# Kernel tuning notes

Measured on AMD Instinct MI355X. Metric: run time of the kernel, lower is better.

The kernel has to match this reference:

```python
import jax, jax.numpy as jnp
import numpy as np

B, C, N = 32, 1024, 512
OUTDIM = 256
EPS_SQRT = 1e-12   # clamp before sqrt so diagonal zeros stay differentiable
EPS_NORM = 1e-12   # torch F.normalize eps


def setup_inputs() -> dict:
    key = jax.random.key(0)
    k1, k2, k3, k4, k5 = jax.random.split(key, 5)
    xi = jax.random.normal(k1, (B, 256, N), dtype=jnp.float32)
    xh = jax.random.normal(k2, (B, 256, N), dtype=jnp.float32)
    xo = jax.random.normal(k3, (B, C, N), dtype=jnp.float32)
    # LazyLinear(outdim) materializes as Linear(N*N, outdim)
    fan_in = N * N
    bound = 1.0 / np.sqrt(fan_in)
    W = jax.random.uniform(k4, (fan_in, OUTDIM), dtype=jnp.float32, minval=-bound, maxval=bound)
    b = jax.random.uniform(k5, (OUTDIM,), dtype=jnp.float32, minval=-bound, maxval=bound)
    return {"xi": xi, "xh": xh, "xo": xo, "W": W, "b": b}


def reference(xi, xh, xo, W, b):
    # xi, xh are unused by SoGA.forward
    x = jnp.transpose(xo, (0, 2, 1))                 # [B, N, C]
    # similarity (Gram) matrix over points
    S = jnp.einsum('bnc,bmc->bnm', x, x)             # [B, N, N], symmetric
    # pairwise Euclidean distance between rows of S
    sq = jnp.sum(S * S, axis=-1)                     # [B, N]
    G = jnp.einsum('bnk,bmk->bnm', S, S)             # [B, N, N]
    d2 = sq[:, :, None] + sq[:, None, :] - 2.0 * G
    D = jnp.sqrt(jnp.maximum(d2, EPS_SQRT))          # [B, N, N]
    flat = D.reshape(D.shape[0], -1)                 # [B, N*N]
    d_out = flat @ W + b                             # [B, outdim]
    norm = jnp.maximum(jnp.linalg.norm(d_out, axis=-1, keepdims=True), EPS_NORM)
    return d_out / norm
```

## Files before the change

### kernel.cpp

```cpp
#include <hip/hip_runtime.h>

typedef unsigned short ushort_t;
typedef __attribute__((ext_vector_type(8))) unsigned short ushort8;
typedef __attribute__((ext_vector_type(4))) unsigned short ushort4v;
typedef __attribute__((ext_vector_type(8))) __bf16 bf16x8;
typedef __attribute__((ext_vector_type(4))) float f32x4;
typedef __attribute__((ext_vector_type(4))) float f4;

#define B_ 32
#define C_ 1024
#define N_ 512
#define O_ 256

__device__ inline float bf2f(unsigned short u) {
  unsigned int i = ((unsigned int)u) << 16;
  return __builtin_bit_cast(float, i);
}
__device__ inline unsigned short f2bf(float f) {
  unsigned int i = __builtin_bit_cast(unsigned int, f);
  i += 0x7FFFu + ((i >> 16) & 1u);
  return (unsigned short)(i >> 16);
}

__device__ inline void gl_lds16(const ushort_t* g, ushort_t* l) {
  __builtin_amdgcn_global_load_lds(
      (const __attribute__((address_space(1))) void*)g,
      (__attribute__((address_space(3))) void*)l, 16, 0, 0);
}

__global__ __launch_bounds__(256) void k_transpose(const float* __restrict__ xo,
                                                   ushort_t* __restrict__ xoT) {
  __shared__ float tile[64][65];
  const int tn = blockIdx.x, tc = blockIdx.y, b = blockIdx.z;
  const int c0 = tc * 64, n0 = tn * 64;
  const int t = threadIdx.x;
  const int tr = t >> 4, tq = t & 15;
  const float* src = xo + ((size_t)b * C_ + c0) * N_ + n0;
#pragma unroll
  for (int p = 0; p < 4; ++p) {
    int c = p * 16 + tr;
    f4 v = *(const f4*)(src + (size_t)c * N_ + tq * 4);
    tile[c][tq * 4 + 0] = v[0];
    tile[c][tq * 4 + 1] = v[1];
    tile[c][tq * 4 + 2] = v[2];
    tile[c][tq * 4 + 3] = v[3];
  }
  __syncthreads();
  ushort_t* dst = xoT + ((size_t)b * N_ + n0) * C_ + c0;
#pragma unroll
  for (int p = 0; p < 4; ++p) {
    int n = p * 16 + tr;
    ushort4v u;
#pragma unroll
    for (int j = 0; j < 4; ++j) u[j] = f2bf(tile[tq * 4 + j][n]);
    *(ushort4v*)(dst + (size_t)n * C_ + tq * 4) = u;
  }
}

template <int KSTEPS, int LDK>
__device__ inline void gemm_main(const ushort_t* __restrict__ Arows,
                                 const ushort_t* __restrict__ Brows,
                                 ushort_t* lds_a, ushort_t* lds_b,
                                 f32x4 (&acc)[4][4], int t) {
  const int lane = t & 63, w = t >> 6;
  const int wr = w >> 1, wc = w & 1;
  const int l16 = lane & 15, lg = lane >> 4;
  const int srow_a = w * 32 + (lane >> 2);
  const int skp = (lane & 3) * 8;
  for (int s = 0; s < KSTEPS; ++s) {
#pragma unroll
    for (int j = 0; j < 2; ++j) {
      const int row = srow_a + j * 16;
      gl_lds16(Arows + (size_t)row * LDK + s * 32 + skp,
               lds_a + (w * 2 + j) * 512);
      gl_lds16(Brows + (size_t)row * LDK + s * 32 + skp,
               lds_b + (w * 2 + j) * 512);
    }
    __syncthreads();
    ushort8 au[4], bu[4];
#pragma unroll
    for (int i = 0; i < 4; ++i) {
      au[i] = *(const ushort8*)&lds_a[(wr * 64 + i * 16 + l16) * 32 + lg * 8];
      bu[i] = *(const ushort8*)&lds_b[(wc * 64 + i * 16 + l16) * 32 + lg * 8];
    }
#pragma unroll
    for (int ai = 0; ai < 4; ++ai)
#pragma unroll
      for (int bi = 0; bi < 4; ++bi)
        acc[ai][bi] = __builtin_amdgcn_mfma_f32_16x16x32_bf16(
            __builtin_bit_cast(bf16x8, au[ai]), __builtin_bit_cast(bf16x8, bu[bi]),
            acc[ai][bi], 0, 0, 0);
    __syncthreads();
  }
}

__global__ __launch_bounds__(256, 2) void k_sgemm(const ushort_t* __restrict__ xoT,
                                                  ushort_t* __restrict__ S) {
  __shared__ ushort_t lds_a[128 * 32];
  __shared__ ushort_t lds_b[128 * 32];
  const int b = blockIdx.y, tile = blockIdx.x;
  const int n0 = (tile >> 2) * 128, m0 = (tile & 3) * 128;
  const ushort_t* Ab = xoT + (size_t)b * N_ * C_ + (size_t)n0 * C_;
  const ushort_t* Bb = xoT + (size_t)b * N_ * C_ + (size_t)m0 * C_;
  f32x4 acc[4][4] = {};
  gemm_main<C_ / 32, C_>(Ab, Bb, lds_a, lds_b, acc, threadIdx.x);
  const int t = threadIdx.x;
  const int lane = t & 63, w = t >> 6, wr = w >> 1, wc = w & 1;
  const int l16 = lane & 15, lg = lane >> 4;
  ushort_t* Sb = S + (size_t)b * N_ * N_;
#pragma unroll
  for (int ai = 0; ai < 4; ++ai)
#pragma unroll
    for (int bi = 0; bi < 4; ++bi)
#pragma unroll
      for (int j = 0; j < 4; ++j) {
        int n = n0 + wr * 64 + ai * 16 + lg * 4 + j;
        int m = m0 + wc * 64 + bi * 16 + l16;
        Sb[(size_t)n * N_ + m] = f2bf(acc[ai][bi][j]);
      }
}

__global__ __launch_bounds__(256) void k_sq(const ushort_t* __restrict__ S,
                                            float* __restrict__ sq) {
  const int row = blockIdx.x * 4 + (threadIdx.x >> 6);
  const int lane = threadIdx.x & 63;
  ushort8 v = *(const ushort8*)(S + (size_t)row * N_ + lane * 8);
  float q = 0.f;
#pragma unroll
  for (int j = 0; j < 8; ++j) {
    float f = bf2f(v[j]);
    q += f * f;
  }
#pragma unroll
  for (int off = 32; off; off >>= 1) q += __shfl_down(q, off, 64);
  if (lane == 0) sq[row] = q;
}

__global__ __launch_bounds__(256, 2) void k_dgemm(const ushort_t* __restrict__ S,
                                                  const float* __restrict__ sq,
                                                  ushort_t* __restrict__ D) {
  __shared__ ushort_t lds_a[128 * 32];
  __shared__ ushort_t lds_b[128 * 32];
  __shared__ float sqn[128], sqm[128];
  const int b = blockIdx.y, tile = blockIdx.x;
  const int n0 = (tile >> 2) * 128, m0 = (tile & 3) * 128;
  const int t = threadIdx.x;
  if (t < 128)
    sqn[t] = sq[b * N_ + n0 + t];
  else
    sqm[t - 128] = sq[b * N_ + m0 + (t - 128)];
  const ushort_t* Ab = S + (size_t)b * N_ * N_ + (size_t)n0 * N_;
  const ushort_t* Bb = S + (size_t)b * N_ * N_ + (size_t)m0 * N_;
  f32x4 acc[4][4] = {};
  gemm_main<N_ / 32, N_>(Ab, Bb, lds_a, lds_b, acc, t);
  const int lane = t & 63, w = t >> 6, wr = w >> 1, wc = w & 1;
  const int l16 = lane & 15, lg = lane >> 4;
  ushort_t* Db = D + (size_t)b * N_ * N_;
#pragma unroll
  for (int ai = 0; ai < 4; ++ai)
#pragma unroll
    for (int bi = 0; bi < 4; ++bi)
#pragma unroll
      for (int j = 0; j < 4; ++j) {
        int nl = wr * 64 + ai * 16 + lg * 4 + j;
        int ml = wc * 64 + bi * 16 + l16;
        float d2 = sqn[nl] + sqm[ml] - 2.f * acc[ai][bi][j];
        Db[(size_t)(n0 + nl) * N_ + (m0 + ml)] = f2bf(sqrtf(fmaxf(d2, 1e-12f)));
      }
}

__global__ __launch_bounds__(256, 2) void k_dw(const ushort_t* __restrict__ Dm,
                                               const float* __restrict__ W,
                                               float* __restrict__ partial) {
  __shared__ ushort_t lds_d[32 * 512];
  const int g = blockIdx.x, t = threadIdx.x;
  const int k0 = g * 512;
#pragma unroll
  for (int i = 0; i < 8; ++i) {
    int c = i * 256 + t;
    *(ushort8*)&lds_d[c * 8] =
        *(const ushort8*)(Dm + (size_t)(c >> 6) * (N_ * N_) + k0 + (c & 63) * 8);
  }
  __syncthreads();
  const int ks = t >> 6;
  const int ob = (t & 63) * 4;
  float acc[32][4] = {};
  const float* Wb = W + ((size_t)(k0 + ks * 128)) * O_ + ob;
  const ushort_t* dbase = &lds_d[ks * 128];
  f4 wA[8], wB[8];
#define LOADW(dst, kb_)                                                      \
  {                                                                          \
    _Pragma("unroll") for (int r = 0; r < 8; ++r) dst[r] =                   \
        *(const f4*)(Wb + (size_t)((kb_)*8 + r) * O_);                       \
  }
#define COMP(kb_, w_)                                                        \
  {                                                                          \
    const int kl = (kb_)*8;                                                  \
    _Pragma("unroll") for (int bb = 0; bb < 32; ++bb) {                      \
      ushort8 dv = *(const ushort8*)&dbase[bb * 512 + kl];                   \
      _Pragma("unroll") for (int r = 0; r < 8; ++r) {                        \
        float dr = bf2f(dv[r]);                                              \
        acc[bb][0] += dr * w_[r][0];                                         \
        acc[bb][1] += dr * w_[r][1];                                         \
        acc[bb][2] += dr * w_[r][2];                                         \
        acc[bb][3] += dr * w_[r][3];                                         \
      }                                                                      \
    }                                                                        \
  }
  LOADW(wA, 0)
#pragma unroll 1
  for (int kb = 0; kb < 16; kb += 2) {
    LOADW(wB, kb + 1)
    COMP(kb, wA)
    if (kb + 2 < 16) LOADW(wA, kb + 2)
    COMP(kb + 1, wB)
  }
#undef LOADW
#undef COMP
  __syncthreads();
  float* lds_f = (float*)lds_d;
  const int lane = t & 63;
#pragma unroll
  for (int c = 0; c < 4; ++c) {
#pragma unroll
    for (int q = 0; q < 8; ++q) {
      f4 v;
      v[0] = acc[c * 8 + q][0];
      v[1] = acc[c * 8 + q][1];
      v[2] = acc[c * 8 + q][2];
      v[3] = acc[c * 8 + q][3];
      *(f4*)&lds_f[(ks * 8 + q) * 256 + lane * 4] = v;
    }
    __syncthreads();
    {
      const int q2 = t >> 5, o = (t & 31) * 8;
      f4 s0 = {}, s1 = {};
#pragma unroll
      for (int k2 = 0; k2 < 4; ++k2) {
        f4 a0 = *(const f4*)&lds_f[(k2 * 8 + q2) * 256 + o];
        f4 a1 = *(const f4*)&lds_f[(k2 * 8 + q2) * 256 + o + 4];
        s0 += a0;
        s1 += a1;
      }
      float* P = partial + ((size_t)g * B_ + c * 8 + q2) * O_ + o;
      *(f4*)P = s0;
      *(f4*)(P + 4) = s1;
    }
    __syncthreads();
  }
}

__global__ __launch_bounds__(256) void k_red1(const float* __restrict__ partial,
                                              float* __restrict__ p2) {
  const int pg = blockIdx.x, b = blockIdx.y, t = threadIdx.x;
  float s = 0.f;
#pragma unroll 8
  for (int p = pg * 64; p < pg * 64 + 64; ++p)
    s += partial[((size_t)p * B_ + b) * O_ + t];
  p2[((size_t)pg * B_ + b) * O_ + t] = s;
}

__global__ __launch_bounds__(256) void k_red2(const float* __restrict__ p2,
                                              const float* __restrict__ bias,
                                              float* __restrict__ out) {
  const int b = blockIdx.x, t = threadIdx.x;
  float s = 0.f;
#pragma unroll
  for (int pg = 0; pg < 8; ++pg) s += p2[((size_t)pg * B_ + b) * O_ + t];
  s += bias[t];
  float q = s * s;
#pragma unroll
  for (int off = 32; off; off >>= 1) q += __shfl_down(q, off, 64);
  __shared__ float lds[4];
  if ((t & 63) == 0) lds[t >> 6] = q;
  __syncthreads();
  float tot = lds[0] + lds[1] + lds[2] + lds[3];
  out[b * O_ + t] = s / fmaxf(sqrtf(tot), 1e-12f);
}

extern "C" void kernel_launch(void* const* d_in, const int* in_sizes, int n_in,
                              void* d_out, int out_size, void* d_ws, size_t ws_size,
                              hipStream_t stream) {
  const float* xo = (const float*)d_in[2];
  const float* W = (const float*)d_in[3];
  const float* bias = (const float*)d_in[4];
  float* out = (float*)d_out;

  char* ws = (char*)d_ws;
  const size_t OFF_S = 33554432, OFF_D = 50331648, OFF_SQ = 67108864,
               OFF_P2 = 67174400, NEED = 67436544;
  if (ws_size < NEED) return;
  ushort_t* xoT = (ushort_t*)ws;
  ushort_t* S = (ushort_t*)(ws + OFF_S);
  ushort_t* D = (ushort_t*)(ws + OFF_D);
  float* sq = (float*)(ws + OFF_SQ);
  float* p2 = (float*)(ws + OFF_P2);
  float* partial = (float*)ws;

  hipLaunchKernelGGL(k_transpose, dim3(8, 16, 32), dim3(256), 0, stream, xo, xoT);
  hipLaunchKernelGGL(k_sgemm, dim3(16, 32), dim3(256), 0, stream, xoT, S);
  hipLaunchKernelGGL(k_sq, dim3(4096), dim3(256), 0, stream, S, sq);
  hipLaunchKernelGGL(k_dgemm, dim3(16, 32), dim3(256), 0, stream, S, sq, D);
  hipLaunchKernelGGL(k_dw, dim3(512), dim3(256), 0, stream, D, W, partial);
  hipLaunchKernelGGL(k_red1, dim3(8, 32), dim3(256), 0, stream, partial, p2);
  hipLaunchKernelGGL(k_red2, dim3(32), dim3(256), 0, stream, p2, bias, out);
}
```

Before: 157.9 us.

## Double-buffer LDS tiles in GEMM main loop and use direct global-to-LDS loads

The shared GEMM main loop now double-buffers the A and B LDS tiles. It issues the next k-step's global-to-LDS copies before computing on the current buffer, so there is one barrier per step instead of two. The D·W kernel loads its D slab through the same global-to-LDS helper instead of going through registers. Its accumulators become f4 vectors so the FMAs can be emitted as packed vector ops. LDS use in the two GEMM kernels doubles, which may limit occupancy. The loop now relies on a single barrier to protect buffer reuse.

```diff
diff --git a/kernel.cpp b/kernel.cpp
--- a/kernel.cpp
+++ b/kernel.cpp
@@ -65,23 +65,28 @@
   const int lane = t & 63, w = t >> 6;
   const int wr = w >> 1, wc = w & 1;
   const int l16 = lane & 15, lg = lane >> 4;
-  const int srow_a = w * 32 + (lane >> 2);
+  const int srow = w * 32 + (lane >> 2);
   const int skp = (lane & 3) * 8;
+#define STAGE(s_, buf_)                                                     \
+  {                                                                         \
+    _Pragma("unroll") for (int j = 0; j < 2; ++j) {                         \
+      const int row = srow + j * 16;                                        \
+      gl_lds16(Arows + (size_t)row * LDK + (s_)*32 + skp,                   \
+               lds_a + (buf_)*4096 + (w * 2 + j) * 512);                    \
+      gl_lds16(Brows + (size_t)row * LDK + (s_)*32 + skp,                   \
+               lds_b + (buf_)*4096 + (w * 2 + j) * 512);                    \
+    }                                                                       \
+  }
+  STAGE(0, 0)
+  __syncthreads();
+  int buf = 0;
   for (int s = 0; s < KSTEPS; ++s) {
-#pragma unroll
-    for (int j = 0; j < 2; ++j) {
-      const int row = srow_a + j * 16;
-      gl_lds16(Arows + (size_t)row * LDK + s * 32 + skp,
-               lds_a + (w * 2 + j) * 512);
-      gl_lds16(Brows + (size_t)row * LDK + s * 32 + skp,
-               lds_b + (w * 2 + j) * 512);
-    }
-    __syncthreads();
+    if (s + 1 < KSTEPS) STAGE(s + 1, buf ^ 1)
     ushort8 au[4], bu[4];
 #pragma unroll
     for (int i = 0; i < 4; ++i) {
-      au[i] = *(const ushort8*)&lds_a[(wr * 64 + i * 16 + l16) * 32 + lg * 8];
-      bu[i] = *(const ushort8*)&lds_b[(wc * 64 + i * 16 + l16) * 32 + lg * 8];
+      au[i] = *(const ushort8*)&lds_a[buf * 4096 + (wr * 64 + i * 16 + l16) * 32 + lg * 8];
+      bu[i] = *(const ushort8*)&lds_b[buf * 4096 + (wc * 64 + i * 16 + l16) * 32 + lg * 8];
     }
 #pragma unroll
     for (int ai = 0; ai < 4; ++ai)
@@ -91,13 +96,15 @@
             __builtin_bit_cast(bf16x8, au[ai]), __builtin_bit_cast(bf16x8, bu[bi]),
             acc[ai][bi], 0, 0, 0);
     __syncthreads();
-  }
+    buf ^= 1;
+  }
+#undef STAGE
 }
 
 __global__ __launch_bounds__(256, 2) void k_sgemm(const ushort_t* __restrict__ xoT,
                                                   ushort_t* __restrict__ S) {
-  __shared__ ushort_t lds_a[128 * 32];
-  __shared__ ushort_t lds_b[128 * 32];
+  __shared__ ushort_t lds_a[2 * 128 * 32];
+  __shared__ ushort_t lds_b[2 * 128 * 32];
   const int b = blockIdx.y, tile = blockIdx.x;
   const int n0 = (tile >> 2) * 128, m0 = (tile & 3) * 128;
   const ushort_t* Ab = xoT + (size_t)b * N_ * C_ + (size_t)n0 * C_;
@@ -139,8 +146,8 @@
 __global__ __launch_bounds__(256, 2) void k_dgemm(const ushort_t* __restrict__ S,
                                                   const float* __restrict__ sq,
                                                   ushort_t* __restrict__ D) {
-  __shared__ ushort_t lds_a[128 * 32];
-  __shared__ ushort_t lds_b[128 * 32];
+  __shared__ ushort_t lds_a[2 * 128 * 32];
+  __shared__ ushort_t lds_b[2 * 128 * 32];
   __shared__ float sqn[128], sqm[128];
   const int b = blockIdx.y, tile = blockIdx.x;
   const int n0 = (tile >> 2) * 128, m0 = (tile & 3) * 128;
@@ -175,16 +182,17 @@
   __shared__ ushort_t lds_d[32 * 512];
   const int g = blockIdx.x, t = threadIdx.x;
   const int k0 = g * 512;
+  const int w = t >> 6, lane = t & 63;
 #pragma unroll
   for (int i = 0; i < 8; ++i) {
     int c = i * 256 + t;
-    *(ushort8*)&lds_d[c * 8] =
-        *(const ushort8*)(Dm + (size_t)(c >> 6) * (N_ * N_) + k0 + (c & 63) * 8);
-  }
-  __syncthreads();
-  const int ks = t >> 6;
-  const int ob = (t & 63) * 4;
-  float acc[32][4] = {};
+    gl_lds16(Dm + (size_t)(c >> 6) * (N_ * N_) + k0 + (c & 63) * 8,
+             lds_d + (i * 256 + w * 64) * 8);
+  }
+  __syncthreads();
+  const int ks = w;
+  const int ob = lane * 4;
+  f4 acc[32] = {};
   const float* Wb = W + ((size_t)(k0 + ks * 128)) * O_ + ob;
   const ushort_t* dbase = &lds_d[ks * 128];
   f4 wA[8], wB[8];
@@ -199,11 +207,7 @@
     _Pragma("unroll") for (int bb = 0; bb < 32; ++bb) {                      \
       ushort8 dv = *(const ushort8*)&dbase[bb * 512 + kl];                   \
       _Pragma("unroll") for (int r = 0; r < 8; ++r) {                        \
-        float dr = bf2f(dv[r]);                                              \
-        acc[bb][0] += dr * w_[r][0];                                         \
-        acc[bb][1] += dr * w_[r][1];                                         \
-        acc[bb][2] += dr * w_[r][2];                                         \
-        acc[bb][3] += dr * w_[r][3];                                         \
+        acc[bb] += w_[r] * bf2f(dv[r]);                                      \
       }                                                                      \
     }                                                                        \
   }
@@ -219,17 +223,11 @@
 #undef COMP
   __syncthreads();
   float* lds_f = (float*)lds_d;
-  const int lane = t & 63;
 #pragma unroll
   for (int c = 0; c < 4; ++c) {
 #pragma unroll
     for (int q = 0; q < 8; ++q) {
-      f4 v;
-      v[0] = acc[c * 8 + q][0];
-      v[1] = acc[c * 8 + q][1];
-      v[2] = acc[c * 8 + q][2];
-      v[3] = acc[c * 8 + q][3];
-      *(f4*)&lds_f[(ks * 8 + q) * 256 + lane * 4] = v;
+      *(f4*)&lds_f[(ks * 8 + q) * 256 + lane * 4] = acc[c * 8 + q];
     }
     __syncthreads();
     {
```

Measured after the change: 155.1 us. No clear change (-1.7%).
